# Kernel tuning notes

Measured on AMD Instinct MI355X. Metric: run time of the kernel, lower is better.

Reference implementation:

```python
import jax, jax.numpy as jnp
import numpy as np

STATE_DIM = 5
OBS_DIM = 32
BATCH = 256
T = 8192


def setup_inputs() -> dict:
    key = jax.random.key(0)
    k1, k2 = jax.random.split(key)
    y = jax.random.normal(k1, (BATCH, T, OBS_DIM), dtype=jnp.float32)
    # parameters as initialized in LGSSM.build()
    A = jnp.eye(STATE_DIM, dtype=jnp.float32) * 0.95
    C = jax.random.normal(k2, (OBS_DIM, STATE_DIM), dtype=jnp.float32) * 0.1
    Q_log_diag = jnp.log(jnp.full((STATE_DIM,), 0.1, dtype=jnp.float32))
    R_log_diag = jnp.log(jnp.full((OBS_DIM,), 0.1, dtype=jnp.float32))
    return {"y": y, "A": A, "C": C, "Q_log_diag": Q_log_diag, "R_log_diag": R_log_diag}


def _kalman_filter(y, A, C, Q, R):
    """Standard Kalman filter over one sequence y: (T, obs_dim).
    Returns filtered states (T, s), covariances (T, s, s), total log-likelihood."""
    s = A.shape[0]
    o = C.shape[0]
    I_s = jnp.eye(s, dtype=y.dtype)
    LOG2PI = jnp.log(jnp.asarray(2.0 * np.pi, dtype=y.dtype))

    def step(carry, y_t):
        z, P = carry
        # predict
        z_pred = A @ z
        P_pred = A @ P @ A.T + Q
        # innovation
        v = y_t - C @ z_pred              # (o,)
        S = C @ P_pred @ C.T + R          # (o, o)
        # Kalman gain K = P_pred C^T S^{-1}
        K = jnp.linalg.solve(S, C @ P_pred).T  # (s, o)
        # update
        z_new = z_pred + K @ v
        P_new = (I_s - K @ C) @ P_pred
        # gaussian log-likelihood of innovation
        Sv = jnp.linalg.solve(S, v)
        _, logdetS = jnp.linalg.slogdet(S)
        ll_t = -0.5 * (o * LOG2PI + logdetS + v @ Sv)
        return (z_new, P_new), (z_new, P_new, ll_t)

    z0 = jnp.zeros((s,), dtype=y.dtype)
    P0 = jnp.eye(s, dtype=y.dtype)
    _, (states, covs, lls) = jax.lax.scan(step, (z0, P0), y)
    return states, covs, jnp.sum(lls)


def reference(y, A, C, Q_log_diag, R_log_diag):
    # diagonal covariances, as in LGSSM.Q / LGSSM.R properties
    Q = jnp.diag(jnp.exp(Q_log_diag))
    R = jnp.diag(jnp.exp(R_log_diag))
    # batch of sequences -> vmap over the independent per-sample filters
    states, covs, ll = jax.vmap(lambda yb: _kalman_filter(yb, A, C, Q, R))(y)
    return states, covs, ll
```

## Files before the change

### kernel.cpp

```cpp
#include <hip/hip_runtime.h>
#include <hip/hip_bf16.h>

#define T_LEN   8192
#define OBS     32
#define SDIM    5
#define NT      64
#define LCHUNK  1024
#define NCHUNK  8
#define WARM    64
#define BATCH   256

#define COVS_OFF  10485760u
#define LL_OFF    62914560u

#define WS_CSUM 0
#define WS_TBL  8

__device__ __forceinline__ float readlane_f(float v, int l) {
  return __int_as_float(__builtin_amdgcn_readlane(__float_as_int(v), l));
}

__global__ void riccati_kernel(const float* __restrict__ Am, const float* __restrict__ Cm,
                               const float* __restrict__ Qld, const float* __restrict__ Rld,
                               float* __restrict__ ws, float* __restrict__ llz)
{
  const int lane = threadIdx.x;
  for (int i = lane; i < BATCH; i += 64) llz[i] = 0.f;

  const int r = (lane < 25) ? (lane / 5) : 0;
  const int c = (lane < 25) ? (lane % 5) : 0;

  float A[25], B[25];
  #pragma unroll
  for (int e = 0; e < 25; ++e) A[e] = Am[e];
  #pragma unroll
  for (int e = 0; e < 25; ++e) B[e] = 0.f;
  float sumR = 0.f;
  for (int o = 0; o < OBS; ++o) {
    const float rl = Rld[o];
    sumR += rl;
    const float rv = expf(-rl);
    float co[5];
    #pragma unroll
    for (int s = 0; s < 5; ++s) co[s] = Cm[o*5+s];
    #pragma unroll
    for (int e = 0; e < 25; ++e) B[e] += rv * co[e/5] * co[e%5];
  }
  const float Qd = expf(Qld[r]);

  float P = (r == c) ? 1.f : 0.f;
  double csum = 0.0;
  float clast = 0.f;
  const float LOG2PI = 1.8378770664093453f;

  for (int t = 0; t < NT; ++t) {
    float U = 0.f;
    #pragma unroll
    for (int k = 0; k < 5; ++k) U += A[r*5+k] * __shfl(P, 5*k+c);
    float Pp = (r == c) ? Qd : 0.f;
    #pragma unroll
    for (int k = 0; k < 5; ++k) Pp += __shfl(U, 5*r+k) * A[c*5+k];
    float M = (r == c) ? 1.f : 0.f;
    #pragma unroll
    for (int k = 0; k < 5; ++k) M += B[r*5+k] * __shfl(Pp, 5*k+c);
    float N = (r == c) ? 1.f : 0.f;
    float logdet = 0.f;
    #pragma unroll
    for (int p = 0; p < 5; ++p) {
      const float piv  = __shfl(M, 6*p);
      const float invp = 1.f / piv;
      logdet += logf(piv);
      const float mp = __shfl(M, 5*p+c) * invp;
      const float np = __shfl(N, 5*p+c) * invp;
      const float f  = __shfl(M, 5*r+p);
      const bool isp = (r == p);
      M = isp ? mp : fmaf(-f, mp, M);
      N = isp ? np : fmaf(-f, np, N);
    }
    float G = 0.f;
    #pragma unroll
    for (int k = 0; k < 5; ++k) G += __shfl(Pp, 5*r+k) * __shfl(N, 5*k+c);
    float W = 0.f;
    #pragma unroll
    for (int k = 0; k < 5; ++k) W += __shfl(G, 5*r+k) * B[k*5+c];
    float Mz = 0.f;
    #pragma unroll
    for (int k = 0; k < 5; ++k) {
      const float X = ((r == k) ? 1.f : 0.f) - __shfl(W, 5*r+k);
      Mz += X * A[k*5+c];
    }
    const float ct = -0.5f * (OBS * LOG2PI + sumR + logdet);
    csum += (double)ct;
    clast = ct;
    if (lane < 25) {
      ws[WS_TBL + t*50 + lane]      = G;
      ws[WS_TBL + t*50 + 25 + lane] = Mz;
    }
    P = G;
  }
  if (lane == 0) ws[WS_CSUM] = (float)(csum + (double)(T_LEN - NT) * (double)clast);
}

__global__ __launch_bounds__(64, 2)
void filter_kernel(const float* __restrict__ y, const float* __restrict__ Am,
                   const float* __restrict__ Cm, const float* __restrict__ Rld,
                   float* __restrict__ out, const float* __restrict__ ws)
{
  const int lane = threadIdx.x;
  const int b  = blockIdx.x >> 3;
  const int ck = blockIdx.x & 7;

  __shared__ float sCw[OBS][SDIM];
  __shared__ float sRinv[OBS];
  __shared__ float sA[25];
  __shared__ float sB[25];
  __shared__ float sMz[NT][25];

  if (lane < OBS) {
    const float rv = expf(-Rld[lane]);
    sRinv[lane] = rv;
    #pragma unroll
    for (int s = 0; s < SDIM; ++s) sCw[lane][s] = Cm[lane*SDIM+s] * rv;
  }
  if (lane < 25) sA[lane] = Am[lane];
  __syncthreads();
  if (lane < 25) {
    const int i = lane / 5, j = lane % 5;
    float acc = 0.f;
    for (int o = 0; o < OBS; ++o) acc += sCw[o][i] * Cm[o*SDIM+j];
    sB[lane] = acc;
  }
  if (ck == 0) {
    for (int idx = lane; idx < NT*25; idx += 64)
      sMz[idx/25][idx%25] = ws[WS_TBL + (idx/25)*50 + 25 + (idx%25)];
  }
  __syncthreads();

  float Gss[25], Mzss[25];
  #pragma unroll
  for (int e = 0; e < 25; ++e) {
    Gss[e]  = ws[WS_TBL + (NT-1)*50 + e];
    Mzss[e] = ws[WS_TBL + (NT-1)*50 + 25 + e];
  }

  const int t0 = ck * LCHUNK;
  const int tstart = (ck == 0) ? 0 : (t0 - WARM);
  const int ngroups = (t0 + LCHUNK - tstart) >> 6;

  const float* yb = y + (size_t)b * T_LEN * OBS;
  float* st = out + (size_t)b * T_LEN * SDIM;
  float* cv = out + (size_t)COVS_OFF + (size_t)b * T_LEN * 25;

  float z[5] = {0,0,0,0,0};
  float llacc = 0.f;

  float4 yv[8], yvn[8];
  {
    const float4* yr = (const float4*)(yb + (size_t)(tstart + lane) * OBS);
    #pragma unroll
    for (int i2 = 0; i2 < 8; ++i2) yv[i2] = yr[i2];
  }

  for (int g = 0; g < ngroups; ++g) {
    const int tb = tstart + (g << 6);
    const int t  = tb + lane;
    const bool post  = (t >= t0);
    const bool trans = (tb < NT);

    {
      const int tn = (g + 1 < ngroups) ? (tb + 64 + lane) : t;
      const float4* yr = (const float4*)(yb + (size_t)tn * OBS);
      #pragma unroll
      for (int i2 = 0; i2 < 8; ++i2) yvn[i2] = yr[i2];
    }

    float u[5] = {0,0,0,0,0};
    float qw = 0.f;
    #pragma unroll
    for (int i2 = 0; i2 < 8; ++i2) {
      const float vals[4] = {yv[i2].x, yv[i2].y, yv[i2].z, yv[i2].w};
      #pragma unroll
      for (int k = 0; k < 4; ++k) {
        const int o = i2*4 + k;
        const float f = vals[k];
        qw = fmaf(sRinv[o]*f, f, qw);
        #pragma unroll
        for (int s = 0; s < 5; ++s) u[s] = fmaf(sCw[o][s], f, u[s]);
      }
    }

    float bvec[5];
    if (trans) {
      const float* Gt = ws + WS_TBL + t*50;
      #pragma unroll
      for (int s = 0; s < 5; ++s) {
        float acc = 0.f;
        #pragma unroll
        for (int k = 0; k < 5; ++k) acc = fmaf(Gt[s*5+k], u[k], acc);
        bvec[s] = acc;
      }
    } else {
      #pragma unroll
      for (int s = 0; s < 5; ++s) {
        float acc = 0.f;
        #pragma unroll
        for (int k = 0; k < 5; ++k) acc = fmaf(Gss[s*5+k], u[k], acc);
        bvec[s] = acc;
      }
    }

    float zprev[5] = {0,0,0,0,0}, znew[5] = {0,0,0,0,0};
    if (!trans) {
      #pragma unroll 8
      for (int j = 0; j < 64; ++j) {
        float nz[5];
        #pragma unroll
        for (int s = 0; s < 5; ++s) {
          float acc = readlane_f(bvec[s], j);
          #pragma unroll
          for (int k = 0; k < 5; ++k) acc = fmaf(Mzss[s*5+k], z[k], acc);
          nz[s] = acc;
        }
        const bool mine = (lane == j);
        #pragma unroll
        for (int s = 0; s < 5; ++s) {
          zprev[s] = mine ? z[s]  : zprev[s];
          znew[s]  = mine ? nz[s] : znew[s];
          z[s] = nz[s];
        }
      }
    } else {
      #pragma unroll 1
      for (int j = 0; j < 64; ++j) {
        float nz[5];
        #pragma unroll
        for (int s = 0; s < 5; ++s) {
          float acc = readlane_f(bvec[s], j);
          #pragma unroll
          for (int k = 0; k < 5; ++k) acc = fmaf(sMz[j][s*5+k], z[k], acc);
          nz[s] = acc;
        }
        const bool mine = (lane == j);
        #pragma unroll
        for (int s = 0; s < 5; ++s) {
          zprev[s] = mine ? z[s]  : zprev[s];
          znew[s]  = mine ? nz[s] : znew[s];
          z[s] = nz[s];
        }
      }
    }

    if (post) {
      float zp[5];
      #pragma unroll
      for (int s = 0; s < 5; ++s) {
        float acc = 0.f;
        #pragma unroll
        for (int k = 0; k < 5; ++k) acc = fmaf(sA[s*5+k], zprev[k], acc);
        zp[s] = acc;
      }
      float w[5], zBz = 0.f, uzp = 0.f;
      #pragma unroll
      for (int s = 0; s < 5; ++s) {
        float bz = 0.f;
        #pragma unroll
        for (int k = 0; k < 5; ++k) bz = fmaf(sB[s*5+k], zp[k], bz);
        w[s] = u[s] - bz;
        zBz = fmaf(zp[s], bz, zBz);
        uzp = fmaf(u[s], zp[s], uzp);
      }
      const float vRv = qw - 2.f*uzp + zBz;
      float wGw = 0.f;
      if (t < NT) {
        const float* Gt = ws + WS_TBL + t*50;
        #pragma unroll
        for (int i2 = 0; i2 < 5; ++i2) {
          #pragma unroll
          for (int k = 0; k < 5; ++k) wGw = fmaf(Gt[i2*5+k]*w[i2], w[k], wGw);
        }
        #pragma unroll
        for (int e = 0; e < 25; ++e) cv[(size_t)t*25 + e] = Gt[e];
      } else {
        #pragma unroll
        for (int i2 = 0; i2 < 5; ++i2) {
          #pragma unroll
          for (int k = 0; k < 5; ++k) wGw = fmaf(Gss[i2*5+k]*w[i2], w[k], wGw);
        }
        #pragma unroll
        for (int e = 0; e < 25; ++e) cv[(size_t)t*25 + e] = Gss[e];
      }
      llacc += (vRv - wGw);
      #pragma unroll
      for (int s = 0; s < 5; ++s) st[(size_t)t*5 + s] = znew[s];
    }

    #pragma unroll
    for (int i2 = 0; i2 < 8; ++i2) yv[i2] = yvn[i2];
  }

  #pragma unroll
  for (int off = 32; off >= 1; off >>= 1) llacc += __shfl_down(llacc, off);
  if (lane == 0) {
    float v = -0.5f * llacc;
    if (ck == 0) v += ws[WS_CSUM];
    atomicAdd(out + (size_t)LL_OFF + b, v);
  }
}

extern "C" void kernel_launch(void* const* d_in, const int* in_sizes, int n_in,
                              void* d_out, int out_size, void* d_ws, size_t ws_size,
                              hipStream_t stream) {
  const float* y   = (const float*)d_in[0];
  const float* A   = (const float*)d_in[1];
  const float* C   = (const float*)d_in[2];
  const float* Qld = (const float*)d_in[3];
  const float* Rld = (const float*)d_in[4];
  float* out = (float*)d_out;
  float* ws  = (float*)d_ws;

  riccati_kernel<<<1, 64, 0, stream>>>(A, C, Qld, Rld, ws, out + (size_t)LL_OFF);
  filter_kernel<<<BATCH*NCHUNK, 64, 0, stream>>>(y, A, C, Rld, out, ws);
}
```

Baseline: 756.7 us.

## Split into 16 chunks, coalesce state/cov stores, simplify scan carry tracking

```diff
diff --git a/kernel.cpp b/kernel.cpp
--- a/kernel.cpp
+++ b/kernel.cpp
@@ -4,9 +4,9 @@
 #define T_LEN   8192
 #define OBS     32
 #define SDIM    5
-#define NT      64
-#define LCHUNK  1024
-#define NCHUNK  8
+#define NT      32
+#define NCHUNK  16
+#define LCHUNK  512
 #define WARM    64
 #define BATCH   256
 
@@ -20,17 +20,15 @@
   return __int_as_float(__builtin_amdgcn_readlane(__float_as_int(v), l));
 }
 
-__global__ void riccati_kernel(const float* __restrict__ Am, const float* __restrict__ Cm,
-                               const float* __restrict__ Qld, const float* __restrict__ Rld,
-                               float* __restrict__ ws, float* __restrict__ llz)
+__global__ __launch_bounds__(64, 1)
+void riccati_kernel(const float* __restrict__ Am, const float* __restrict__ Cm,
+                    const float* __restrict__ Qld, const float* __restrict__ Rld,
+                    float* __restrict__ ws, float* __restrict__ llz)
 {
   const int lane = threadIdx.x;
   for (int i = lane; i < BATCH; i += 64) llz[i] = 0.f;
 
-  const int r = (lane < 25) ? (lane / 5) : 0;
-  const int c = (lane < 25) ? (lane % 5) : 0;
-
-  float A[25], B[25];
+  float A[25], B[25], P[25];
   #pragma unroll
   for (int e = 0; e < 25; ++e) A[e] = Am[e];
   #pragma unroll
@@ -44,95 +42,145 @@
     #pragma unroll
     for (int s = 0; s < 5; ++s) co[s] = Cm[o*5+s];
     #pragma unroll
-    for (int e = 0; e < 25; ++e) B[e] += rv * co[e/5] * co[e%5];
-  }
-  const float Qd = expf(Qld[r]);
-
-  float P = (r == c) ? 1.f : 0.f;
-  double csum = 0.0;
-  float clast = 0.f;
+    for (int i = 0; i < 5; ++i)
+      #pragma unroll
+      for (int j = 0; j < 5; ++j) B[i*5+j] = fmaf(rv*co[i], co[j], B[i*5+j]);
+  }
+  float Qd[5];
+  #pragma unroll
+  for (int s = 0; s < 5; ++s) Qd[s] = expf(Qld[s]);
+  #pragma unroll
+  for (int e = 0; e < 25; ++e) P[e] = (e % 6 == 0) ? 1.f : 0.f;
+
+  double csum = 0.0; float clast = 0.f;
   const float LOG2PI = 1.8378770664093453f;
 
   for (int t = 0; t < NT; ++t) {
-    float U = 0.f;
-    #pragma unroll
-    for (int k = 0; k < 5; ++k) U += A[r*5+k] * __shfl(P, 5*k+c);
-    float Pp = (r == c) ? Qd : 0.f;
-    #pragma unroll
-    for (int k = 0; k < 5; ++k) Pp += __shfl(U, 5*r+k) * A[c*5+k];
-    float M = (r == c) ? 1.f : 0.f;
-    #pragma unroll
-    for (int k = 0; k < 5; ++k) M += B[r*5+k] * __shfl(Pp, 5*k+c);
-    float N = (r == c) ? 1.f : 0.f;
+    float U[25], Pp[25], M[25], N[25], G[25];
+    #pragma unroll
+    for (int i = 0; i < 5; ++i)
+      #pragma unroll
+      for (int j = 0; j < 5; ++j) {
+        float acc = 0.f;
+        #pragma unroll
+        for (int k = 0; k < 5; ++k) acc = fmaf(A[i*5+k], P[k*5+j], acc);
+        U[i*5+j] = acc;
+      }
+    #pragma unroll
+    for (int i = 0; i < 5; ++i)
+      #pragma unroll
+      for (int j = 0; j < 5; ++j) {
+        float acc = (i == j) ? Qd[i] : 0.f;
+        #pragma unroll
+        for (int k = 0; k < 5; ++k) acc = fmaf(U[i*5+k], A[j*5+k], acc);
+        Pp[i*5+j] = acc;
+      }
+    #pragma unroll
+    for (int i = 0; i < 5; ++i)
+      #pragma unroll
+      for (int j = 0; j < 5; ++j) {
+        float acc = (i == j) ? 1.f : 0.f;
+        #pragma unroll
+        for (int k = 0; k < 5; ++k) acc = fmaf(B[i*5+k], Pp[k*5+j], acc);
+        M[i*5+j] = acc;
+      }
+    #pragma unroll
+    for (int e = 0; e < 25; ++e) N[e] = (e % 6 == 0) ? 1.f : 0.f;
     float logdet = 0.f;
     #pragma unroll
     for (int p = 0; p < 5; ++p) {
-      const float piv  = __shfl(M, 6*p);
-      const float invp = 1.f / piv;
+      const float piv = M[p*5+p];
+      const float ip  = 1.f / piv;
       logdet += logf(piv);
-      const float mp = __shfl(M, 5*p+c) * invp;
-      const float np = __shfl(N, 5*p+c) * invp;
-      const float f  = __shfl(M, 5*r+p);
-      const bool isp = (r == p);
-      M = isp ? mp : fmaf(-f, mp, M);
-      N = isp ? np : fmaf(-f, np, N);
-    }
-    float G = 0.f;
-    #pragma unroll
-    for (int k = 0; k < 5; ++k) G += __shfl(Pp, 5*r+k) * __shfl(N, 5*k+c);
-    float W = 0.f;
-    #pragma unroll
-    for (int k = 0; k < 5; ++k) W += __shfl(G, 5*r+k) * B[k*5+c];
-    float Mz = 0.f;
-    #pragma unroll
-    for (int k = 0; k < 5; ++k) {
-      const float X = ((r == k) ? 1.f : 0.f) - __shfl(W, 5*r+k);
-      Mz += X * A[k*5+c];
+      #pragma unroll
+      for (int j = 0; j < 5; ++j) { M[p*5+j] *= ip; N[p*5+j] *= ip; }
+      #pragma unroll
+      for (int r2 = 0; r2 < 5; ++r2) if (r2 != p) {
+        const float f = M[r2*5+p];
+        #pragma unroll
+        for (int j = 0; j < 5; ++j) {
+          M[r2*5+j] = fmaf(-f, M[p*5+j], M[r2*5+j]);
+          N[r2*5+j] = fmaf(-f, N[p*5+j], N[r2*5+j]);
+        }
+      }
+    }
+    #pragma unroll
+    for (int i = 0; i < 5; ++i)
+      #pragma unroll
+      for (int j = 0; j < 5; ++j) {
+        float acc = 0.f;
+        #pragma unroll
+        for (int k = 0; k < 5; ++k) acc = fmaf(Pp[i*5+k], N[k*5+j], acc);
+        G[i*5+j] = acc;
+      }
+    #pragma unroll
+    for (int i = 0; i < 5; ++i) {
+      float Wr[5];
+      #pragma unroll
+      for (int j = 0; j < 5; ++j) {
+        float acc = 0.f;
+        #pragma unroll
+        for (int k = 0; k < 5; ++k) acc = fmaf(G[i*5+k], B[k*5+j], acc);
+        Wr[j] = acc;
+      }
+      #pragma unroll
+      for (int j = 0; j < 5; ++j) {
+        float acc = A[i*5+j];
+        #pragma unroll
+        for (int k = 0; k < 5; ++k) acc = fmaf(-Wr[k], A[k*5+j], acc);
+        if (lane == 0) ws[WS_TBL + t*50 + 25 + i*5 + j] = acc;
+      }
+    }
+    if (lane == 0) {
+      #pragma unroll
+      for (int e = 0; e < 25; ++e) ws[WS_TBL + t*50 + e] = G[e];
     }
     const float ct = -0.5f * (OBS * LOG2PI + sumR + logdet);
-    csum += (double)ct;
-    clast = ct;
-    if (lane < 25) {
-      ws[WS_TBL + t*50 + lane]      = G;
-      ws[WS_TBL + t*50 + 25 + lane] = Mz;
-    }
-    P = G;
+    csum += (double)ct; clast = ct;
+    #pragma unroll
+    for (int e = 0; e < 25; ++e) P[e] = G[e];
   }
   if (lane == 0) ws[WS_CSUM] = (float)(csum + (double)(T_LEN - NT) * (double)clast);
 }
 
-__global__ __launch_bounds__(64, 2)
+__global__ __launch_bounds__(64, 4)
 void filter_kernel(const float* __restrict__ y, const float* __restrict__ Am,
                    const float* __restrict__ Cm, const float* __restrict__ Rld,
                    float* __restrict__ out, const float* __restrict__ ws)
 {
   const int lane = threadIdx.x;
-  const int b  = blockIdx.x >> 3;
-  const int ck = blockIdx.x & 7;
-
-  __shared__ float sCw[OBS][SDIM];
-  __shared__ float sRinv[OBS];
+  const int b  = blockIdx.x >> 4;
+  const int ck = blockIdx.x & 15;
+
+  __shared__ float sCwr[OBS][8];
   __shared__ float sA[25];
   __shared__ float sB[25];
-  __shared__ float sMz[NT][25];
+  __shared__ float sG[25];
+  __shared__ float sMz[64][25];
+  __shared__ float zbuf[64*5];
 
   if (lane < OBS) {
     const float rv = expf(-Rld[lane]);
-    sRinv[lane] = rv;
-    #pragma unroll
-    for (int s = 0; s < SDIM; ++s) sCw[lane][s] = Cm[lane*SDIM+s] * rv;
+    sCwr[lane][5] = rv;
+    #pragma unroll
+    for (int s = 0; s < SDIM; ++s) sCwr[lane][s] = Cm[lane*SDIM+s] * rv;
   }
   if (lane < 25) sA[lane] = Am[lane];
   __syncthreads();
   if (lane < 25) {
     const int i = lane / 5, j = lane % 5;
     float acc = 0.f;
-    for (int o = 0; o < OBS; ++o) acc += sCw[o][i] * Cm[o*SDIM+j];
+    for (int o = 0; o < OBS; ++o) acc = fmaf(sCwr[o][i], Cm[o*SDIM+j], acc);
     sB[lane] = acc;
+    sG[lane] = ws[WS_TBL + (NT-1)*50 + lane];
   }
   if (ck == 0) {
-    for (int idx = lane; idx < NT*25; idx += 64)
-      sMz[idx/25][idx%25] = ws[WS_TBL + (idx/25)*50 + 25 + (idx%25)];
+    for (int it = 0; it < 25; ++it) {
+      const int idx = lane + 64*it;
+      const int tt = idx / 25, e = idx % 25;
+      const int ts = (tt < NT) ? tt : (NT-1);
+      sMz[tt][e] = ws[WS_TBL + ts*50 + 25 + e];
+    }
   }
   __syncthreads();
 
@@ -151,151 +199,162 @@
   float* st = out + (size_t)b * T_LEN * SDIM;
   float* cv = out + (size_t)COVS_OFF + (size_t)b * T_LEN * 25;
 
-  float z[5] = {0,0,0,0,0};
+  float zc[5] = {0,0,0,0,0};
   float llacc = 0.f;
 
-  float4 yv[8], yvn[8];
+  float4 yv[8];
   {
     const float4* yr = (const float4*)(yb + (size_t)(tstart + lane) * OBS);
     #pragma unroll
     for (int i2 = 0; i2 < 8; ++i2) yv[i2] = yr[i2];
   }
+
+  const int e0 = lane - (lane >= 50 ? 50 : (lane >= 25 ? 25 : 0));
 
   for (int g = 0; g < ngroups; ++g) {
     const int tb = tstart + (g << 6);
     const int t  = tb + lane;
-    const bool post  = (t >= t0);
-    const bool trans = (tb < NT);
-
-    {
-      const int tn = (g + 1 < ngroups) ? (tb + 64 + lane) : t;
-      const float4* yr = (const float4*)(yb + (size_t)tn * OBS);
-      #pragma unroll
-      for (int i2 = 0; i2 < 8; ++i2) yvn[i2] = yr[i2];
-    }
+    const bool warm   = (tb < t0);
+    const bool transG = (ck == 0) && (g == 0);
 
     float u[5] = {0,0,0,0,0};
     float qw = 0.f;
     #pragma unroll
-    for (int i2 = 0; i2 < 8; ++i2) {
-      const float vals[4] = {yv[i2].x, yv[i2].y, yv[i2].z, yv[i2].w};
-      #pragma unroll
-      for (int k = 0; k < 4; ++k) {
-        const int o = i2*4 + k;
-        const float f = vals[k];
-        qw = fmaf(sRinv[o]*f, f, qw);
-        #pragma unroll
-        for (int s = 0; s < 5; ++s) u[s] = fmaf(sCw[o][s], f, u[s]);
-      }
+    for (int o = 0; o < OBS; ++o) {
+      const float f = ((const float*)yv)[o];
+      const float4 cw4 = *(const float4*)&sCwr[o][0];
+      const float2 cw2 = *(const float2*)&sCwr[o][4];
+      qw  = fmaf(cw2.y * f, f, qw);
+      u[0] = fmaf(cw4.x, f, u[0]);
+      u[1] = fmaf(cw4.y, f, u[1]);
+      u[2] = fmaf(cw4.z, f, u[2]);
+      u[3] = fmaf(cw4.w, f, u[3]);
+      u[4] = fmaf(cw2.x, f, u[4]);
+    }
+
+    if (g + 1 < ngroups) {
+      const float4* yr = (const float4*)(yb + (size_t)(tb + 64 + lane) * OBS);
+      #pragma unroll
+      for (int i2 = 0; i2 < 8; ++i2) yv[i2] = yr[i2];
     }
 
     float bvec[5];
-    if (trans) {
-      const float* Gt = ws + WS_TBL + t*50;
-      #pragma unroll
-      for (int s = 0; s < 5; ++s) {
-        float acc = 0.f;
-        #pragma unroll
-        for (int k = 0; k < 5; ++k) acc = fmaf(Gt[s*5+k], u[k], acc);
-        bvec[s] = acc;
+    if (!transG) {
+      #pragma unroll
+      for (int s2 = 0; s2 < 5; ++s2) {
+        float acc = 0.f;
+        #pragma unroll
+        for (int k = 0; k < 5; ++k) acc = fmaf(Gss[s2*5+k], u[k], acc);
+        bvec[s2] = acc;
       }
     } else {
-      #pragma unroll
-      for (int s = 0; s < 5; ++s) {
-        float acc = 0.f;
-        #pragma unroll
-        for (int k = 0; k < 5; ++k) acc = fmaf(Gss[s*5+k], u[k], acc);
-        bvec[s] = acc;
-      }
-    }
-
-    float zprev[5] = {0,0,0,0,0}, znew[5] = {0,0,0,0,0};
-    if (!trans) {
+      const float* gp = ws + WS_TBL + (size_t)((t < NT) ? t : (NT-1)) * 50;
+      #pragma unroll
+      for (int s2 = 0; s2 < 5; ++s2) {
+        float acc = 0.f;
+        #pragma unroll
+        for (int k = 0; k < 5; ++k) acc = fmaf(gp[s2*5+k], u[k], acc);
+        bvec[s2] = acc;
+      }
+    }
+
+    float z[5];
+    #pragma unroll
+    for (int s2 = 0; s2 < 5; ++s2) z[s2] = zc[s2];
+    if (!transG) {
       #pragma unroll 8
       for (int j = 0; j < 64; ++j) {
         float nz[5];
         #pragma unroll
-        for (int s = 0; s < 5; ++s) {
-          float acc = readlane_f(bvec[s], j);
+        for (int s2 = 0; s2 < 5; ++s2) {
+          float acc = readlane_f(bvec[s2], j);
           #pragma unroll
-          for (int k = 0; k < 5; ++k) acc = fmaf(Mzss[s*5+k], z[k], acc);
-          nz[s] = acc;
+          for (int k = 0; k < 5; ++k) acc = fmaf(Mzss[s2*5+k], z[k], acc);
+          nz[s2] = acc;
         }
-        const bool mine = (lane == j);
-        #pragma unroll
-        for (int s = 0; s < 5; ++s) {
-          zprev[s] = mine ? z[s]  : zprev[s];
-          znew[s]  = mine ? nz[s] : znew[s];
-          z[s] = nz[s];
-        }
+        #pragma unroll
+        for (int s2 = 0; s2 < 5; ++s2) z[s2] = (lane >= j) ? nz[s2] : z[s2];
       }
     } else {
-      #pragma unroll 1
+      #pragma unroll 4
       for (int j = 0; j < 64; ++j) {
         float nz[5];
         #pragma unroll
-        for (int s = 0; s < 5; ++s) {
-          float acc = readlane_f(bvec[s], j);
+        for (int s2 = 0; s2 < 5; ++s2) {
+          float acc = readlane_f(bvec[s2], j);
           #pragma unroll
-          for (int k = 0; k < 5; ++k) acc = fmaf(sMz[j][s*5+k], z[k], acc);
-          nz[s] = acc;
+          for (int k = 0; k < 5; ++k) acc = fmaf(sMz[j][s2*5+k], z[k], acc);
+          nz[s2] = acc;
         }
-        const bool mine = (lane == j);
-        #pragma unroll
-        for (int s = 0; s < 5; ++s) {
-          zprev[s] = mine ? z[s]  : zprev[s];
-          znew[s]  = mine ? nz[s] : znew[s];
-          z[s] = nz[s];
-        }
-      }
-    }
-
-    if (post) {
+        #pragma unroll
+        for (int s2 = 0; s2 < 5; ++s2) z[s2] = (lane >= j) ? nz[s2] : z[s2];
+      }
+    }
+
+    float zprev[5];
+    #pragma unroll
+    for (int s2 = 0; s2 < 5; ++s2) {
+      const float v = __shfl_up(z[s2], 1);
+      zprev[s2] = (lane == 0) ? zc[s2] : v;
+    }
+    #pragma unroll
+    for (int s2 = 0; s2 < 5; ++s2) zc[s2] = readlane_f(z[s2], 63);
+
+    if (!warm) {
       float zp[5];
       #pragma unroll
-      for (int s = 0; s < 5; ++s) {
-        float acc = 0.f;
-        #pragma unroll
-        for (int k = 0; k < 5; ++k) acc = fmaf(sA[s*5+k], zprev[k], acc);
-        zp[s] = acc;
+      for (int s2 = 0; s2 < 5; ++s2) {
+        float acc = 0.f;
+        #pragma unroll
+        for (int k = 0; k < 5; ++k) acc = fmaf(sA[s2*5+k], zprev[k], acc);
+        zp[s2] = acc;
       }
       float w[5], zBz = 0.f, uzp = 0.f;
       #pragma unroll
-      for (int s = 0; s < 5; ++s) {
+      for (int s2 = 0; s2 < 5; ++s2) {
         float bz = 0.f;
         #pragma unroll
-        for (int k = 0; k < 5; ++k) bz = fmaf(sB[s*5+k], zp[k], bz);
-        w[s] = u[s] - bz;
-        zBz = fmaf(zp[s], bz, zBz);
-        uzp = fmaf(u[s], zp[s], uzp);
+        for (int k = 0; k < 5; ++k) bz = fmaf(sB[s2*5+k], zp[k], bz);
+        w[s2] = u[s2] - bz;
+        zBz = fmaf(zp[s2], bz, zBz);
+        uzp = fmaf(u[s2], zp[s2], uzp);
       }
       const float vRv = qw - 2.f*uzp + zBz;
       float wGw = 0.f;
-      if (t < NT) {
-        const float* Gt = ws + WS_TBL + t*50;
-        #pragma unroll
-        for (int i2 = 0; i2 < 5; ++i2) {
-          #pragma unroll
-          for (int k = 0; k < 5; ++k) wGw = fmaf(Gt[i2*5+k]*w[i2], w[k], wGw);
-        }
-        #pragma unroll
-        for (int e = 0; e < 25; ++e) cv[(size_t)t*25 + e] = Gt[e];
-      } else {
-        #pragma unroll
-        for (int i2 = 0; i2 < 5; ++i2) {
+      if (!transG) {
+        #pragma unroll
+        for (int i2 = 0; i2 < 5; ++i2)
           #pragma unroll
           for (int k = 0; k < 5; ++k) wGw = fmaf(Gss[i2*5+k]*w[i2], w[k], wGw);
+      } else {
+        const float* gp = ws + WS_TBL + (size_t)((t < NT) ? t : (NT-1)) * 50;
+        #pragma unroll
+        for (int i2 = 0; i2 < 5; ++i2)
+          #pragma unroll
+          for (int k = 0; k < 5; ++k) wGw = fmaf(gp[i2*5+k]*w[i2], w[k], wGw);
+      }
+      llacc += vRv - wGw;
+
+      #pragma unroll
+      for (int s2 = 0; s2 < 5; ++s2) zbuf[lane*5 + s2] = z[s2];
+      float* stg = st + (size_t)tb * 5;
+      #pragma unroll
+      for (int k = 0; k < 5; ++k) stg[lane + 64*k] = zbuf[lane + 64*k];
+
+      if (!transG) {
+        float* cvg = cv + (size_t)tb * 25;
+        int e = e0;
+        #pragma unroll
+        for (int k = 0; k < 25; ++k) {
+          cvg[lane + 64*k] = sG[e];
+          e += 14; if (e >= 25) e -= 25;
         }
-        #pragma unroll
-        for (int e = 0; e < 25; ++e) cv[(size_t)t*25 + e] = Gss[e];
-      }
-      llacc += (vRv - wGw);
-      #pragma unroll
-      for (int s = 0; s < 5; ++s) st[(size_t)t*5 + s] = znew[s];
-    }
-
-    #pragma unroll
-    for (int i2 = 0; i2 < 8; ++i2) yv[i2] = yvn[i2];
+      } else {
+        const float* gp = ws + WS_TBL + (size_t)((t < NT) ? t : (NT-1)) * 50;
+        #pragma unroll
+        for (int e = 0; e < 25; ++e) cv[(size_t)t*25 + e] = gp[e];
+      }
+    }
   }
 
   #pragma unroll
```

Result: slower. 1.019 ms (+34.6%).
